# Kernel optimization log

Hardware: AMD Instinct MI355X
Metric: run time of the kernel (lower is better)

Reference implementation:

```python
import jax, jax.numpy as jnp
import numpy as np

C = 0.11512925464970229  # ln(10)/20
K = 15
FD = 128
FS = 160
OV = 40
MAX_LAG = 256
PAD_L = K // 2
PAD_R = K - 1 - PAD_L
LOG_GAIN_LIMIT = 10 * C
GAIN_A = (6.0 * C - (-6.0 * C)) / 2
GAIN_B = (6.0 * C + (-6.0 * C)) / 2


def setup_inputs() -> dict:
    key = jax.random.key(0)
    ks = jax.random.split(key, 8)
    B, NF = 32, 500
    N = NF * FS
    x = jax.random.normal(ks[0], (B, 1, N), dtype=jnp.float32)
    features = jax.random.normal(ks[1], (B, NF, FD), dtype=jnp.float32)
    lags = jax.random.randint(ks[2], (B, NF), 0, 256)
    s = 1.0 / np.sqrt(FD)
    ck_w = jax.random.normal(ks[3], (K, FD), dtype=jnp.float32) * s
    ck_b = jax.random.normal(ks[4], (K,), dtype=jnp.float32) * 0.01
    fg_w = jax.random.normal(ks[5], (1, FD), dtype=jnp.float32) * s
    fg_b = jnp.full((1,), max(0.1, 4.0 + LOG_GAIN_LIMIT), dtype=jnp.float32)
    gg_w = jax.random.normal(ks[6], (1, FD), dtype=jnp.float32) * s
    gg_b = jax.random.normal(ks[7], (1,), dtype=jnp.float32) * 0.01
    return {"x": x, "features": features, "lags": lags,
            "ck_w": ck_w, "ck_b": ck_b, "fg_w": fg_w, "fg_b": fg_b,
            "gg_w": gg_w, "gg_b": gg_b}


def reference(x, features, lags, ck_w, ck_b, fg_w, fg_b, gg_w, gg_b):
    B, _, N = x.shape
    NF = features.shape[1]
    OUT = FS + OV  # per-frame output length before crossfade

    # per-frame FIR kernels, p=2 normalized over taps
    kernels = jnp.einsum('bfd,kd->bfk', features, ck_w) + ck_b          # (B,NF,K)
    kernels = kernels / (1e-6 + jnp.sqrt(jnp.sum(kernels**2, -1, keepdims=True)))
    # per-frame scalar gains
    gains = jnp.exp(-jax.nn.relu(features @ fg_w[0] + fg_b[0]) + LOG_GAIN_LIMIT)   # (B,NF)
    ggains = jnp.exp(GAIN_A * jnp.tanh(features @ gg_w[0] + gg_b[0]) + GAIN_B)     # (B,NF)

    # pad: [PAD_L,PAD_R] for conv, then [MAX_LAG, OV] for lag gather / final frame
    xp = jnp.pad(x[:, 0, :], ((0, 0), (MAX_LAG + PAD_L, PAD_R + OV)))   # (B,Np)

    L = FS + K - 1 + OV
    t = jnp.arange(L)
    f_off = jnp.arange(NF) * FS
    cidx = t[None, None, :] + f_off[None, :, None] + MAX_LAG - lags[:, :, None]  # (B,NF,L)
    xx = xp[jnp.arange(B)[:, None, None], cidx]                         # (B,NF,L)

    # grouped conv1d == cross-correlation with per-frame kernel
    win = jnp.stack([xx[:, :, k:k + OUT] for k in range(K)], axis=-1)   # (B,NF,OUT,K)
    conv = jnp.einsum('bflk,bfk->bfl', win, kernels)                    # (B,NF,OUT)

    # dry path
    offset = MAX_LAG + PAD_L
    pt_idx = offset + f_off[:, None] + jnp.arange(OUT)[None, :]         # (NF,OUT)
    pt = xp[:, pt_idx]                                                  # (B,NF,OUT)

    new_chunk = ggains[:, :, None] * (conv * gains[:, :, None] + pt)    # (B,NF,OUT)

    # overlap-add crossfade between consecutive frames
    win2 = 0.5 + 0.5 * jnp.cos((jnp.arange(OV) + 0.5) * jnp.pi / OV)
    win1 = win2[::-1]
    tails = new_chunk[:, :, FS:]                                        # (B,NF,OV)
    prev = jnp.concatenate([jnp.zeros_like(tails[:, :1]), tails[:, :-1]], axis=1)
    head = new_chunk[:, :, :OV] * win1 + prev * win2
    out = jnp.concatenate([head, new_chunk[:, :, OV:FS]], axis=-1)      # (B,NF,FS)
    return out.reshape(B, 1, NF * FS)
```

## Files before the change

kernel.cpp:

```cpp
#include <hip/hip_runtime.h>
#include <math.h>

namespace {
constexpr int K = 15;
constexpr int FD = 128;
constexpr int FS = 160;
constexpr int OV = 40;
constexpr int NFRAMES = 500;
constexpr int NSAMP = NFRAMES * FS;
constexpr float C_CONST = 0.11512925464970229f;
constexpr float LOG_GAIN_LIMIT = 10.0f * C_CONST;
constexpr float GAIN_A = 6.0f * C_CONST;
constexpr int FPB = 10;
constexpr int NFR = FPB + 1;
constexpr int NW4 = 55;
constexpr int WINA = 220;
constexpr int SFSTR = 132;
constexpr float PI_F = 3.14159265358979323846f;
}

__global__ __launch_bounds__(256)
void comb_fused(const float* __restrict__ x,
                const float* __restrict__ feat,
                const int*   __restrict__ lags,
                const float* __restrict__ ck_w,
                const float* __restrict__ ck_b,
                const float* __restrict__ fg_w,
                const float* __restrict__ fg_b,
                const float* __restrict__ gg_w,
                const float* __restrict__ gg_b,
                float* __restrict__ out)
{
    const int tid = threadIdx.x;
    const int bid = blockIdx.x;
    const int b   = bid / (NFRAMES / FPB);
    const int blk = bid - b * (NFRAMES / FPB);
    const int f0  = blk * FPB;

    __shared__ __align__(16) float sf[NFR][SFSTR];
    __shared__ __align__(16) float swin[NFR][WINA];
    __shared__ float sdots[NFR][17];
    __shared__ __align__(16) float sfk[NFR][16];
    __shared__ __align__(16) float swin2[OV + 8];

    const float* xb = x + (size_t)b * NSAMP;

    for (int i = tid; i < NFR * (FD / 4); i += 256) {
        const int fr = i >> 5;
        const int e4 = i & 31;
        const int pf = f0 - 1 + fr;
        float4 v = make_float4(0.f, 0.f, 0.f, 0.f);
        if (pf >= 0)
            v = ((const float4*)feat)[((size_t)b * NFRAMES + pf) * (FD / 4) + e4];
        *(float4*)&sf[fr][e4 * 4] = v;
    }

    for (int i = tid; i < NFR * NW4; i += 256) {
        const int fr = i / NW4;
        const int m  = i - fr * NW4;
        const int pf = f0 - 1 + fr;
        float4 v = make_float4(0.f, 0.f, 0.f, 0.f);
        if (pf >= 0) {
            const int base = pf * FS - lags[b * NFRAMES + pf] - 7;
            const int idx  = base + 4 * m;
            if (idx >= 0 && idx + 3 < NSAMP) {
                v = *(const float4*)(xb + idx);
            } else {
                if (idx     >= 0 && idx     < NSAMP) v.x = xb[idx];
                if (idx + 1 >= 0 && idx + 1 < NSAMP) v.y = xb[idx + 1];
                if (idx + 2 >= 0 && idx + 2 < NSAMP) v.z = xb[idx + 2];
                if (idx + 3 >= 0 && idx + 3 < NSAMP) v.w = xb[idx + 3];
            }
        }
        *(float4*)&swin[fr][4 * m] = v;
    }

    if (tid < OV)
        swin2[tid] = 0.5f + 0.5f * cosf(((float)tid + 0.5f) * (PI_F / OV));
    __syncthreads();

    if (tid < NFR * 17) {
        const int fr = tid / 17;
        const int j  = tid - fr * 17;
        const float* wrow = (j < K) ? (ck_w + (size_t)j * FD)
                                    : ((j == K) ? fg_w : gg_w);
        const float4* w4 = (const float4*)wrow;
        const float4* f4 = (const float4*)&sf[fr][0];
        float4 acc = make_float4(0.f, 0.f, 0.f, 0.f);
        #pragma unroll
        for (int i = 0; i < FD / 4; ++i) {
            const float4 a = f4[i];
            const float4 w = w4[i];
            acc.x += a.x * w.x; acc.y += a.y * w.y;
            acc.z += a.z * w.z; acc.w += a.w * w.w;
        }
        const float bias = (j < K) ? ck_b[j] : ((j == K) ? fg_b[0] : gg_b[0]);
        sdots[fr][j] = acc.x + acc.y + acc.z + acc.w + bias;
    }
    __syncthreads();

    if (tid < NFR) {
        const int pf = f0 - 1 + tid;
        if (pf < 0) {
            #pragma unroll
            for (int k = 0; k < 16; ++k) sfk[tid][k] = 0.f;
        } else {
            float kern[K];
            float n2 = 0.f;
            #pragma unroll
            for (int k = 0; k < K; ++k) {
                kern[k] = sdots[tid][k];
                n2 += kern[k] * kern[k];
            }
            const float inv   = 1.f / (1e-6f + sqrtf(n2));
            const float gain  = expf(-fmaxf(sdots[tid][K], 0.f) + LOG_GAIN_LIMIT);
            const float ggain = expf(GAIN_A * tanhf(sdots[tid][K + 1]));
            const float ks    = ggain * gain * inv;
            #pragma unroll
            for (int k = 0; k < K; ++k) sfk[tid][k] = ks * kern[k];
            sfk[tid][15] = ggain;
        }
    }
    __syncthreads();

    const int obase = f0 * FS;
    for (int g = tid; g < FPB * (FS / 4); g += 256) {
        const int frl = g / (FS / 4);
        const int gi  = g - frl * (FS / 4);
        const int t   = gi * 4;
        const int fr  = frl + 1;

        const float4 k0 = *(const float4*)&sfk[fr][0];
        const float4 k1 = *(const float4*)&sfk[fr][4];
        const float4 k2 = *(const float4*)&sfk[fr][8];
        const float4 k3 = *(const float4*)&sfk[fr][12];
        const float kc[16] = {k0.x,k0.y,k0.z,k0.w, k1.x,k1.y,k1.z,k1.w,
                              k2.x,k2.y,k2.z,k2.w, k3.x,k3.y,k3.z,k3.w};

        float w[20];
        #pragma unroll
        for (int q = 0; q < 5; ++q)
            *(float4*)&w[4 * q] = *(const float4*)&swin[fr][t + 4 * q];

        const float4 pt = *(const float4*)(xb + obase + frl * FS + t);

        float4 res;
        {
            float c0 = 0.f, c1 = 0.f, c2 = 0.f, c3 = 0.f;
            #pragma unroll
            for (int k = 0; k < K; ++k) {
                const float kk = kc[k];
                c0 += w[k]     * kk;
                c1 += w[k + 1] * kk;
                c2 += w[k + 2] * kk;
                c3 += w[k + 3] * kk;
            }
            const float ps = kc[15];
            res.x = c0 + ps * pt.x; res.y = c1 + ps * pt.y;
            res.z = c2 + ps * pt.z; res.w = c3 + ps * pt.w;
        }

        if (gi < OV / 4) {
            const float4 q0 = *(const float4*)&sfk[fr - 1][0];
            const float4 q1 = *(const float4*)&sfk[fr - 1][4];
            const float4 q2 = *(const float4*)&sfk[fr - 1][8];
            const float4 q3 = *(const float4*)&sfk[fr - 1][12];
            const float qc[16] = {q0.x,q0.y,q0.z,q0.w, q1.x,q1.y,q1.z,q1.w,
                                  q2.x,q2.y,q2.z,q2.w, q3.x,q3.y,q3.z,q3.w};
            float wv[20];
            #pragma unroll
            for (int q = 0; q < 5; ++q)
                *(float4*)&wv[4 * q] = *(const float4*)&swin[fr - 1][FS + t + 4 * q];

            float c0 = 0.f, c1 = 0.f, c2 = 0.f, c3 = 0.f;
            #pragma unroll
            for (int k = 0; k < K; ++k) {
                const float kk = qc[k];
                c0 += wv[k]     * kk;
                c1 += wv[k + 1] * kk;
                c2 += wv[k + 2] * kk;
                c3 += wv[k + 3] * kk;
            }
            const float ps = qc[15];
            const float4 tail = make_float4(c0 + ps * pt.x, c1 + ps * pt.y,
                                            c2 + ps * pt.z, c3 + ps * pt.w);
            const float4 w2 = *(const float4*)&swin2[t];
            res.x = res.x * (1.f - w2.x) + tail.x * w2.x;
            res.y = res.y * (1.f - w2.y) + tail.y * w2.y;
            res.z = res.z * (1.f - w2.z) + tail.z * w2.z;
            res.w = res.w * (1.f - w2.w) + tail.w * w2.w;
        }

        *(float4*)(out + (size_t)b * NSAMP + obase + frl * FS + t) = res;
    }
}

extern "C" void kernel_launch(void* const* d_in, const int* in_sizes, int n_in,
                              void* d_out, int out_size, void* d_ws, size_t ws_size,
                              hipStream_t stream) {
    const float* x    = (const float*)d_in[0];
    const float* feat = (const float*)d_in[1];
    const int*   lags = (const int*)d_in[2];
    const float* ck_w = (const float*)d_in[3];
    const float* ck_b = (const float*)d_in[4];
    const float* fg_w = (const float*)d_in[5];
    const float* fg_b = (const float*)d_in[6];
    const float* gg_w = (const float*)d_in[7];
    const float* gg_b = (const float*)d_in[8];
    float* out = (float*)d_out;

    const int B = in_sizes[0] / NSAMP;
    const int nblocks = B * (NFRAMES / FPB);
    comb_fused<<<dim3(nblocks), dim3(256), 0, stream>>>(
        x, feat, lags, ck_w, ck_b, fg_w, fg_b, gg_w, gg_b, out);
}
```

Measured before the change: 106.4 us.

## Split per-frame parameter projection into separate kernel before synthesis

Moves the feature-to-kernel/gain projection into its own kernel that writes 16 floats per frame to workspace, and the synthesis kernel then reads those parameters. The fused version recomputed one extra frame's projection per block (11 of every 10 frames) and held feature data in shared memory, which increased LDS use and lengthened the serial phase before synthesis could start. The split adds a second launch and a round trip of the parameters through global memory.

```diff
diff --git a/kernel.cpp b/kernel.cpp
--- a/kernel.cpp
+++ b/kernel.cpp
@@ -11,25 +11,96 @@
 constexpr float C_CONST = 0.11512925464970229f;
 constexpr float LOG_GAIN_LIMIT = 10.0f * C_CONST;
 constexpr float GAIN_A = 6.0f * C_CONST;
+constexpr float PI_F = 3.14159265358979323846f;
+
+constexpr int K1FPB = 15;
+constexpr int SFSTR = 132;
+
 constexpr int FPB = 10;
 constexpr int NFR = FPB + 1;
 constexpr int NW4 = 55;
 constexpr int WINA = 220;
-constexpr int SFSTR = 132;
-constexpr float PI_F = 3.14159265358979323846f;
 }
 
 __global__ __launch_bounds__(256)
-void comb_fused(const float* __restrict__ x,
-                const float* __restrict__ feat,
-                const int*   __restrict__ lags,
-                const float* __restrict__ ck_w,
-                const float* __restrict__ ck_b,
-                const float* __restrict__ fg_w,
-                const float* __restrict__ fg_b,
-                const float* __restrict__ gg_w,
-                const float* __restrict__ gg_b,
-                float* __restrict__ out)
+void params_kernel(const float* __restrict__ feat,
+                   const float* __restrict__ ck_w,
+                   const float* __restrict__ ck_b,
+                   const float* __restrict__ fg_w,
+                   const float* __restrict__ fg_b,
+                   const float* __restrict__ gg_w,
+                   const float* __restrict__ gg_b,
+                   float* __restrict__ params,
+                   int G)
+{
+    const int tid = threadIdx.x;
+    const int g0  = blockIdx.x * K1FPB;
+
+    __shared__ __align__(16) float sfeat[K1FPB][SFSTR];
+    __shared__ float sdots[K1FPB][17];
+
+    for (int i = tid; i < K1FPB * (FD / 4); i += 256) {
+        const int fi = i >> 5;
+        const int e4 = i & 31;
+        const int g  = g0 + fi;
+        float4 v = make_float4(0.f, 0.f, 0.f, 0.f);
+        if (g < G) v = ((const float4*)feat)[(size_t)g * (FD / 4) + e4];
+        *(float4*)&sfeat[fi][e4 * 4] = v;
+    }
+    __syncthreads();
+
+    if (tid < K1FPB * 17) {
+        const int fi = tid / 17;
+        const int j  = tid - fi * 17;
+        const float* wrow = (j < K) ? (ck_w + (size_t)j * FD)
+                                    : ((j == K) ? fg_w : gg_w);
+        const float4* w4 = (const float4*)wrow;
+        const float4* f4 = (const float4*)&sfeat[fi][0];
+        float4 acc = make_float4(0.f, 0.f, 0.f, 0.f);
+        #pragma unroll
+        for (int i = 0; i < FD / 4; ++i) {
+            const float4 a = f4[i];
+            const float4 w = w4[i];
+            acc.x += a.x * w.x; acc.y += a.y * w.y;
+            acc.z += a.z * w.z; acc.w += a.w * w.w;
+        }
+        const float bias = (j < K) ? ck_b[j] : ((j == K) ? fg_b[0] : gg_b[0]);
+        sdots[fi][j] = acc.x + acc.y + acc.z + acc.w + bias;
+    }
+    __syncthreads();
+
+    if (tid < K1FPB) {
+        const int g = g0 + tid;
+        if (g < G) {
+            float kern[K];
+            float n2 = 0.f;
+            #pragma unroll
+            for (int k = 0; k < K; ++k) {
+                kern[k] = sdots[tid][k];
+                n2 += kern[k] * kern[k];
+            }
+            const float inv   = 1.f / (1e-6f + sqrtf(n2));
+            const float gain  = expf(-fmaxf(sdots[tid][K], 0.f) + LOG_GAIN_LIMIT);
+            const float ggain = expf(GAIN_A * tanhf(sdots[tid][K + 1]));
+            const float ks    = ggain * gain * inv;
+            float p[16];
+            #pragma unroll
+            for (int k = 0; k < K; ++k) p[k] = ks * kern[k];
+            p[15] = ggain;
+            float4* dst = (float4*)(params + (size_t)g * 16);
+            dst[0] = *(float4*)&p[0];
+            dst[1] = *(float4*)&p[4];
+            dst[2] = *(float4*)&p[8];
+            dst[3] = *(float4*)&p[12];
+        }
+    }
+}
+
+__global__ __launch_bounds__(256)
+void synth_kernel(const float* __restrict__ x,
+                  const int*   __restrict__ lags,
+                  const float* __restrict__ params,
+                  float* __restrict__ out)
 {
     const int tid = threadIdx.x;
     const int bid = blockIdx.x;
@@ -37,23 +108,11 @@
     const int blk = bid - b * (NFRAMES / FPB);
     const int f0  = blk * FPB;
 
-    __shared__ __align__(16) float sf[NFR][SFSTR];
     __shared__ __align__(16) float swin[NFR][WINA];
-    __shared__ float sdots[NFR][17];
     __shared__ __align__(16) float sfk[NFR][16];
     __shared__ __align__(16) float swin2[OV + 8];
 
     const float* xb = x + (size_t)b * NSAMP;
-
-    for (int i = tid; i < NFR * (FD / 4); i += 256) {
-        const int fr = i >> 5;
-        const int e4 = i & 31;
-        const int pf = f0 - 1 + fr;
-        float4 v = make_float4(0.f, 0.f, 0.f, 0.f);
-        if (pf >= 0)
-            v = ((const float4*)feat)[((size_t)b * NFRAMES + pf) * (FD / 4) + e4];
-        *(float4*)&sf[fr][e4 * 4] = v;
-    }
 
     for (int i = tid; i < NFR * NW4; i += 256) {
         const int fr = i / NW4;
@@ -75,51 +134,19 @@
         *(float4*)&swin[fr][4 * m] = v;
     }
 
-    if (tid < OV)
-        swin2[tid] = 0.5f + 0.5f * cosf(((float)tid + 0.5f) * (PI_F / OV));
-    __syncthreads();
-
-    if (tid < NFR * 17) {
-        const int fr = tid / 17;
-        const int j  = tid - fr * 17;
-        const float* wrow = (j < K) ? (ck_w + (size_t)j * FD)
-                                    : ((j == K) ? fg_w : gg_w);
-        const float4* w4 = (const float4*)wrow;
-        const float4* f4 = (const float4*)&sf[fr][0];
-        float4 acc = make_float4(0.f, 0.f, 0.f, 0.f);
-        #pragma unroll
-        for (int i = 0; i < FD / 4; ++i) {
-            const float4 a = f4[i];
-            const float4 w = w4[i];
-            acc.x += a.x * w.x; acc.y += a.y * w.y;
-            acc.z += a.z * w.z; acc.w += a.w * w.w;
-        }
-        const float bias = (j < K) ? ck_b[j] : ((j == K) ? fg_b[0] : gg_b[0]);
-        sdots[fr][j] = acc.x + acc.y + acc.z + acc.w + bias;
-    }
-    __syncthreads();
-
-    if (tid < NFR) {
-        const int pf = f0 - 1 + tid;
-        if (pf < 0) {
-            #pragma unroll
-            for (int k = 0; k < 16; ++k) sfk[tid][k] = 0.f;
-        } else {
-            float kern[K];
-            float n2 = 0.f;
-            #pragma unroll
-            for (int k = 0; k < K; ++k) {
-                kern[k] = sdots[tid][k];
-                n2 += kern[k] * kern[k];
-            }
-            const float inv   = 1.f / (1e-6f + sqrtf(n2));
-            const float gain  = expf(-fmaxf(sdots[tid][K], 0.f) + LOG_GAIN_LIMIT);
-            const float ggain = expf(GAIN_A * tanhf(sdots[tid][K + 1]));
-            const float ks    = ggain * gain * inv;
-            #pragma unroll
-            for (int k = 0; k < K; ++k) sfk[tid][k] = ks * kern[k];
-            sfk[tid][15] = ggain;
-        }
+    if (tid < NFR * 4) {
+        const int fr = tid >> 2;
+        const int q  = tid & 3;
+        const int pf = f0 - 1 + fr;
+        float4 v = make_float4(0.f, 0.f, 0.f, 0.f);
+        if (pf >= 0)
+            v = ((const float4*)(params + ((size_t)b * NFRAMES + pf) * 16))[q];
+        *(float4*)&sfk[fr][q * 4] = v;
+    }
+
+    if (tid >= 64 && tid < 64 + OV) {
+        const int t = tid - 64;
+        swin2[t] = 0.5f + 0.5f * cosf(((float)t + 0.5f) * (PI_F / OV));
     }
     __syncthreads();
 
@@ -207,10 +234,17 @@
     const float* fg_b = (const float*)d_in[6];
     const float* gg_w = (const float*)d_in[7];
     const float* gg_b = (const float*)d_in[8];
-    float* out = (float*)d_out;
+    float* out    = (float*)d_out;
+    float* params = (float*)d_ws;
 
     const int B = in_sizes[0] / NSAMP;
-    const int nblocks = B * (NFRAMES / FPB);
-    comb_fused<<<dim3(nblocks), dim3(256), 0, stream>>>(
-        x, feat, lags, ck_w, ck_b, fg_w, fg_b, gg_w, gg_b, out);
-}
+    const int G = B * NFRAMES;
+
+    const int nblk1 = (G + K1FPB - 1) / K1FPB;
+    params_kernel<<<dim3(nblk1), dim3(256), 0, stream>>>(
+        feat, ck_w, ck_b, fg_w, fg_b, gg_w, gg_b, params, G);
+
+    const int nblk2 = B * (NFRAMES / FPB);
+    synth_kernel<<<dim3(nblk2), dim3(256), 0, stream>>>(
+        x, lags, params, out);
+}
```

Result: slower. 110.1 us (+3.5%).
